# Optimization experiments

Measured on AMD Instinct MI355X. Metric: run time of the kernel, lower is better.

Reference implementation:

```python
import jax, jax.numpy as jnp
import numpy as np
from jax import lax


def setup_inputs() -> dict:
    key = jax.random.key(0)
    k1, k2 = jax.random.split(key)
    B, C = 128, 256
    z_f = jax.random.normal(k1, (B, C, 7, 7), dtype=jnp.float32)
    x_f = jax.random.normal(k2, (B, C, 31, 31), dtype=jnp.float32)
    return {"z_f": z_f, "x_f": x_f}


def xcorr_depthwise(search, kernel):
    # search: [B, C, Hx, Wx], kernel: [B, C, Hz, Wz]
    B, C, Hx, Wx = search.shape
    _, _, Hz, Wz = kernel.shape
    s = search.reshape(1, B * C, Hx, Wx)          # [1, B*C, Hx, Wx]
    k = kernel.reshape(B * C, 1, Hz, Wz)          # [B*C, 1, Hz, Wz]
    out = lax.conv_general_dilated(
        s, k,
        window_strides=(1, 1),
        padding='VALID',
        dimension_numbers=('NCHW', 'OIHW', 'NCHW'),
        feature_group_count=B * C,
    )                                             # [1, B*C, Ho, Wo]
    Ho, Wo = Hx - Hz + 1, Wx - Wz + 1
    return out.reshape(B, C, Ho, Wo)


def reference(z_f, x_f):
    # DepthwiseRPN.forward: xcorr_depthwise(search=x_f, kernel=z_f)
    return xcorr_depthwise(x_f, z_f)
```

## Files before the change

kernel.cpp:

```cpp
#include <hip/hip_runtime.h>


#define PPB 5
#define WX 31
#define XPLANE 961
#define TDW (PPB * XPLANE)
#define LPLANE 1024
#define XREG (PPB * LPLANE)
#define ZPLANE 49
#define ZDW (PPB * ZPLANE)
#define ZREG 256
#define OPLANE 625
#define WO 25

typedef __attribute__((address_space(1))) const void gaddr_t;
typedef __attribute__((address_space(3))) void laddr_t;

__global__ __launch_bounds__(128, 2) void dwxcorr_kernel(
    const float* __restrict__ z, const float* __restrict__ x,
    float* __restrict__ out, int nplanes) {
  __shared__ float lds[XREG + ZREG];

  const int tid = threadIdx.x;
  const int t = blockIdx.x;
  const int wb4 = (tid & ~63) * 4;
  const int wb1 = tid & ~63;
  const long XTOT = (long)nplanes * XPLANE;
  const long ZTOT = (long)nplanes * ZPLANE;
  const long xoff = (long)t * TDW;
  const long zoff = (long)t * ZDW;
  const long gz0 = zoff & ~3L;
  const int offz = (int)(zoff & 3);

  if (xoff + TDW + 31 <= XTOT && gz0 + ZREG <= ZTOT) {
#pragma unroll
    for (int c = 0; c < 10; ++c) {
      int s = c * 512 + tid * 4;
      int p = s >> 10;
      int row = (s >> 5) & 31;
      int q = s & 31;
      int qq = q ^ ((row & 7) << 2);
      long g = xoff + p * XPLANE + row * WX + qq;
      __builtin_amdgcn_global_load_lds((gaddr_t*)(x + g),
                                       (laddr_t*)&lds[c * 512 + wb4], 16, 0, 0);
    }
    if (tid < 63)
      __builtin_amdgcn_global_load_lds((gaddr_t*)(z + gz0 + tid * 4),
                                       (laddr_t*)&lds[XREG + wb4], 16, 0, 0);
  } else {
#pragma unroll
    for (int c = 0; c < 40; ++c) {
      int s = c * 128 + tid;
      int p = s >> 10;
      int row = (s >> 5) & 31;
      int q = s & 31;
      int qq = q ^ ((row & 7) << 2);
      long g = xoff + p * XPLANE + row * WX + qq;
      if (g > XTOT - 1) g = XTOT - 1;
      __builtin_amdgcn_global_load_lds((gaddr_t*)(x + g),
                                       (laddr_t*)&lds[c * 128 + wb1], 4, 0, 0);
    }
    if (tid < 63) {
      long gz = gz0 + tid * 4;
      if (gz > ZTOT - 4) gz = ZTOT - 4;
      __builtin_amdgcn_global_load_lds((gaddr_t*)(z + gz),
                                       (laddr_t*)&lds[XREG + wb4], 16, 0, 0);
    }
  }
  __syncthreads();

  const int p0 = t * PPB;
  const int pmax = min(PPB, nplanes - p0);
  const int cpp = tid / 25;
  if (tid >= PPB * 25 || cpp >= pmax) return;
  const int t25 = tid - cpp * 25;
  const int ty = t25 / 5;
  const int tx = t25 - ty * 5;
  const int tx5 = tx * 5;

  const float* zb = &lds[XREG + offz + cpp * ZPLANE];
  float zr[ZPLANE];
#pragma unroll
  for (int j = 0; j < ZPLANE; ++j) zr[j] = zb[j];

  float acc[5][5];
#pragma unroll
  for (int r = 0; r < 5; ++r)
#pragma unroll
    for (int j = 0; j < 5; ++j) acc[r][j] = 0.0f;

  const float* pb = &lds[cpp * LPLANE];

#pragma unroll
  for (int iy = 0; iy < 11; ++iy) {
    const int row = ty * 5 + iy;
    const int rb = row << 5;
    const int f = (row & 7) << 2;
    float xr[11];
#pragma unroll
    for (int k = 0; k < 11; ++k) xr[k] = pb[rb + ((tx5 + k) ^ f)];
    const int ky_lo = (iy - 4 < 0) ? 0 : iy - 4;
    const int ky_hi = (iy < 6) ? iy : 6;
#pragma unroll
    for (int ky = 0; ky < 7; ++ky) {
      if (ky < ky_lo || ky > ky_hi) continue;
      const int orow = iy - ky;
#pragma unroll
      for (int kx = 0; kx < 7; ++kx) {
        const float zv = zr[ky * 7 + kx];
#pragma unroll
        for (int j = 0; j < 5; ++j)
          acc[orow][j] = fmaf(xr[kx + j], zv, acc[orow][j]);
      }
    }
  }

  float* ob = out + (long)(p0 + cpp) * OPLANE + (ty * 5) * WO + tx5;
#pragma unroll
  for (int r = 0; r < 5; ++r)
#pragma unroll
    for (int j = 0; j < 5; ++j) ob[r * WO + j] = acc[r][j];
}

extern "C" void kernel_launch(void* const* d_in, const int* in_sizes, int n_in,
                              void* d_out, int out_size, void* d_ws, size_t ws_size,
                              hipStream_t stream) {
  const float* z = (const float*)d_in[0];
  const float* x = (const float*)d_in[1];
  float* out = (float*)d_out;

  const int nplanes = in_sizes[0] / ZPLANE;
  const int blocks = (nplanes + PPB - 1) / PPB;

  hipLaunchKernelGGL(dwxcorr_kernel, dim3(blocks), dim3(128), 0, stream,
                     z, x, out, nplanes);
}
```

Baseline: 45.47 us.

## Assign one full output row per thread with vectorized row loads

Each thread now computes a whole 25-wide output row instead of a 5x5 tile. It loads each of the 7 needed input rows as eight float4 LDS reads, undoing the XOR swizzle at chunk granularity. Filter weights are read from LDS per tap rather than held in 49 registers. This cuts total LDS read instructions, but threads now read full rows with more redundancy across output rows, and stores become 25 contiguous floats per thread, which may coalesce worse.

```diff
diff --git a/kernel.cpp b/kernel.cpp
--- a/kernel.cpp
+++ b/kernel.cpp
@@ -73,53 +73,40 @@
   const int pmax = min(PPB, nplanes - p0);
   const int cpp = tid / 25;
   if (tid >= PPB * 25 || cpp >= pmax) return;
-  const int t25 = tid - cpp * 25;
-  const int ty = t25 / 5;
-  const int tx = t25 - ty * 5;
-  const int tx5 = tx * 5;
+  const int oy = tid - cpp * 25;
 
   const float* zb = &lds[XREG + offz + cpp * ZPLANE];
-  float zr[ZPLANE];
+
+  float acc[25];
 #pragma unroll
-  for (int j = 0; j < ZPLANE; ++j) zr[j] = zb[j];
-
-  float acc[5][5];
-#pragma unroll
-  for (int r = 0; r < 5; ++r)
-#pragma unroll
-    for (int j = 0; j < 5; ++j) acc[r][j] = 0.0f;
-
-  const float* pb = &lds[cpp * LPLANE];
+  for (int j = 0; j < 25; ++j) acc[j] = 0.0f;
 
 #pragma unroll
-  for (int iy = 0; iy < 11; ++iy) {
-    const int row = ty * 5 + iy;
-    const int rb = row << 5;
-    const int f = (row & 7) << 2;
-    float xr[11];
+  for (int ky = 0; ky < 7; ++ky) {
+    const int row = oy + ky;
+    const int rf = row & 7;
+    const float4* rp = (const float4*)&lds[(cpp << 10) | (row << 5)];
+    float rowbuf[32];
 #pragma unroll
-    for (int k = 0; k < 11; ++k) xr[k] = pb[rb + ((tx5 + k) ^ f)];
-    const int ky_lo = (iy - 4 < 0) ? 0 : iy - 4;
-    const int ky_hi = (iy < 6) ? iy : 6;
+    for (int c = 0; c < 8; ++c) {
+      float4 v = rp[c ^ rf];
+      rowbuf[c * 4 + 0] = v.x;
+      rowbuf[c * 4 + 1] = v.y;
+      rowbuf[c * 4 + 2] = v.z;
+      rowbuf[c * 4 + 3] = v.w;
+    }
 #pragma unroll
-    for (int ky = 0; ky < 7; ++ky) {
-      if (ky < ky_lo || ky > ky_hi) continue;
-      const int orow = iy - ky;
+    for (int kx = 0; kx < 7; ++kx) {
+      const float zv = zb[ky * 7 + kx];
 #pragma unroll
-      for (int kx = 0; kx < 7; ++kx) {
-        const float zv = zr[ky * 7 + kx];
-#pragma unroll
-        for (int j = 0; j < 5; ++j)
-          acc[orow][j] = fmaf(xr[kx + j], zv, acc[orow][j]);
-      }
+      for (int ox = 0; ox < 25; ++ox)
+        acc[ox] = fmaf(rowbuf[ox + kx], zv, acc[ox]);
     }
   }
 
-  float* ob = out + (long)(p0 + cpp) * OPLANE + (ty * 5) * WO + tx5;
+  float* ob = out + (long)(p0 + cpp) * OPLANE + oy * WO;
 #pragma unroll
-  for (int r = 0; r < 5; ++r)
-#pragma unroll
-    for (int j = 0; j < 5; ++j) ob[r * WO + j] = acc[r][j];
+  for (int j = 0; j < 25; ++j) ob[j] = acc[j];
 }
 
 extern "C" void kernel_launch(void* const* d_in, const int* in_sizes, int n_in,
```

After: 56.04 us. 23.2% more time.

## Convert to persistent grid with register-staged prefetch of next tile

Applied to the files above, without the earlier changes.

Launches a fixed grid of 1792 blocks that loop over plane tiles instead of one block per tile. The next tile's x and z data are loaded from global memory into registers while the current tile is computed from LDS, then written to LDS after a barrier. The goal is to hide global load latency behind compute. The cost is 40 extra registers per thread for staging, which may hurt occupancy under launch_bounds(128,2), and it replaces the direct global-to-LDS loads with plain global loads followed by LDS stores.

```diff
diff --git a/kernel.cpp b/kernel.cpp
--- a/kernel.cpp
+++ b/kernel.cpp
@@ -12,114 +12,130 @@
 #define ZREG 256
 #define OPLANE 625
 #define WO 25
-
-typedef __attribute__((address_space(1))) const void gaddr_t;
-typedef __attribute__((address_space(3))) void laddr_t;
+#define GRID 1792
 
 __global__ __launch_bounds__(128, 2) void dwxcorr_kernel(
     const float* __restrict__ z, const float* __restrict__ x,
-    float* __restrict__ out, int nplanes) {
+    float* __restrict__ out, int nplanes, int ntiles) {
   __shared__ float lds[XREG + ZREG];
 
   const int tid = threadIdx.x;
-  const int t = blockIdx.x;
-  const int wb4 = (tid & ~63) * 4;
-  const int wb1 = tid & ~63;
   const long XTOT = (long)nplanes * XPLANE;
   const long ZTOT = (long)nplanes * ZPLANE;
-  const long xoff = (long)t * TDW;
-  const long zoff = (long)t * ZDW;
-  const long gz0 = zoff & ~3L;
-  const int offz = (int)(zoff & 3);
 
-  if (xoff + TDW + 31 <= XTOT && gz0 + ZREG <= ZTOT) {
+  int soff[10];
+#pragma unroll
+  for (int c = 0; c < 10; ++c) {
+    int s = c * 512 + tid * 4;
+    int p = s >> 10;
+    int row = (s >> 5) & 31;
+    int q = s & 31;
+    int qq = q ^ ((row & 7) << 2);
+    soff[c] = p * XPLANE + row * WX + qq;
+  }
+
+  float xrs[40];
+  float4 zr4 = make_float4(0.f, 0.f, 0.f, 0.f);
+
+  auto LOADT = [&](int t) {
+    const long xoff = (long)t * TDW;
+    const long gz0 = ((long)t * ZDW) & ~3L;
+    if (xoff + TDW + 31 <= XTOT && gz0 + ZREG <= ZTOT) {
+#pragma unroll
+      for (int c = 0; c < 10; ++c) {
+        const float* gp = x + xoff + soff[c];
+#pragma unroll
+        for (int j = 0; j < 4; ++j) xrs[c * 4 + j] = gp[j];
+      }
+      if (tid < 63) zr4 = *(const float4*)(z + gz0 + tid * 4);
+    } else {
+#pragma unroll
+      for (int c = 0; c < 10; ++c) {
+#pragma unroll
+        for (int j = 0; j < 4; ++j) {
+          long gj = xoff + soff[c] + j;
+          if (gj > XTOT - 1) gj = XTOT - 1;
+          xrs[c * 4 + j] = x[gj];
+        }
+      }
+      if (tid < 63) {
+        long gz = gz0 + tid * 4;
+        if (gz > ZTOT - 4) gz = ZTOT - 4;
+        zr4 = *(const float4*)(z + gz);
+      }
+    }
+  };
+
+  const int bstart = blockIdx.x;
+  LOADT(bstart);
+
+  for (int t = bstart; t < ntiles; t += GRID) {
+    __syncthreads();
 #pragma unroll
     for (int c = 0; c < 10; ++c) {
-      int s = c * 512 + tid * 4;
-      int p = s >> 10;
-      int row = (s >> 5) & 31;
-      int q = s & 31;
-      int qq = q ^ ((row & 7) << 2);
-      long g = xoff + p * XPLANE + row * WX + qq;
-      __builtin_amdgcn_global_load_lds((gaddr_t*)(x + g),
-                                       (laddr_t*)&lds[c * 512 + wb4], 16, 0, 0);
+      float4 v = make_float4(xrs[c * 4 + 0], xrs[c * 4 + 1],
+                             xrs[c * 4 + 2], xrs[c * 4 + 3]);
+      *(float4*)&lds[c * 512 + tid * 4] = v;
     }
-    if (tid < 63)
-      __builtin_amdgcn_global_load_lds((gaddr_t*)(z + gz0 + tid * 4),
-                                       (laddr_t*)&lds[XREG + wb4], 16, 0, 0);
-  } else {
+    if (tid < 63) *(float4*)&lds[XREG + tid * 4] = zr4;
+    __syncthreads();
+
+    const int tn = t + GRID;
+    if (tn < ntiles) LOADT(tn);
+
+    const int p0 = t * PPB;
+    const int pmax = min(PPB, nplanes - p0);
+    const int cpp = tid / 25;
+    if (tid < PPB * 25 && cpp < pmax) {
+      const int t25 = tid - cpp * 25;
+      const int ty = t25 / 5;
+      const int tx = t25 - ty * 5;
+      const int tx5 = tx * 5;
+      const int offz = (int)(((long)t * ZDW) & 3);
+
+      const float* zb = &lds[XREG + offz + cpp * ZPLANE];
+      float zr[ZPLANE];
 #pragma unroll
-    for (int c = 0; c < 40; ++c) {
-      int s = c * 128 + tid;
-      int p = s >> 10;
-      int row = (s >> 5) & 31;
-      int q = s & 31;
-      int qq = q ^ ((row & 7) << 2);
-      long g = xoff + p * XPLANE + row * WX + qq;
-      if (g > XTOT - 1) g = XTOT - 1;
-      __builtin_amdgcn_global_load_lds((gaddr_t*)(x + g),
-                                       (laddr_t*)&lds[c * 128 + wb1], 4, 0, 0);
-    }
-    if (tid < 63) {
-      long gz = gz0 + tid * 4;
-      if (gz > ZTOT - 4) gz = ZTOT - 4;
-      __builtin_amdgcn_global_load_lds((gaddr_t*)(z + gz),
-                                       (laddr_t*)&lds[XREG + wb4], 16, 0, 0);
+      for (int j = 0; j < ZPLANE; ++j) zr[j] = zb[j];
+
+      float acc[5][5];
+#pragma unroll
+      for (int r = 0; r < 5; ++r)
+#pragma unroll
+        for (int j2 = 0; j2 < 5; ++j2) acc[r][j2] = 0.0f;
+
+      const float* pb = &lds[cpp * LPLANE];
+#pragma unroll
+      for (int iy = 0; iy < 11; ++iy) {
+        const int row = ty * 5 + iy;
+        const int rb = row << 5;
+        const int f = (row & 7) << 2;
+        float xr[11];
+#pragma unroll
+        for (int k = 0; k < 11; ++k) xr[k] = pb[rb + ((tx5 + k) ^ f)];
+        const int ky_lo = (iy - 4 < 0) ? 0 : iy - 4;
+        const int ky_hi = (iy < 6) ? iy : 6;
+#pragma unroll
+        for (int ky = 0; ky < 7; ++ky) {
+          if (ky < ky_lo || ky > ky_hi) continue;
+          const int orow = iy - ky;
+#pragma unroll
+          for (int kx = 0; kx < 7; ++kx) {
+            const float zv = zr[ky * 7 + kx];
+#pragma unroll
+            for (int j2 = 0; j2 < 5; ++j2)
+              acc[orow][j2] = fmaf(xr[kx + j2], zv, acc[orow][j2]);
+          }
+        }
+      }
+
+      float* ob = out + (long)(p0 + cpp) * OPLANE + (ty * 5) * WO + tx5;
+#pragma unroll
+      for (int r = 0; r < 5; ++r)
+#pragma unroll
+        for (int j2 = 0; j2 < 5; ++j2) ob[r * WO + j2] = acc[r][j2];
     }
   }
-  __syncthreads();
-
-  const int p0 = t * PPB;
-  const int pmax = min(PPB, nplanes - p0);
-  const int cpp = tid / 25;
-  if (tid >= PPB * 25 || cpp >= pmax) return;
-  const int t25 = tid - cpp * 25;
-  const int ty = t25 / 5;
-  const int tx = t25 - ty * 5;
-  const int tx5 = tx * 5;
-
-  const float* zb = &lds[XREG + offz + cpp * ZPLANE];
-  float zr[ZPLANE];
-#pragma unroll
-  for (int j = 0; j < ZPLANE; ++j) zr[j] = zb[j];
-
-  float acc[5][5];
-#pragma unroll
-  for (int r = 0; r < 5; ++r)
-#pragma unroll
-    for (int j = 0; j < 5; ++j) acc[r][j] = 0.0f;
-
-  const float* pb = &lds[cpp * LPLANE];
-
-#pragma unroll
-  for (int iy = 0; iy < 11; ++iy) {
-    const int row = ty * 5 + iy;
-    const int rb = row << 5;
-    const int f = (row & 7) << 2;
-    float xr[11];
-#pragma unroll
-    for (int k = 0; k < 11; ++k) xr[k] = pb[rb + ((tx5 + k) ^ f)];
-    const int ky_lo = (iy - 4 < 0) ? 0 : iy - 4;
-    const int ky_hi = (iy < 6) ? iy : 6;
-#pragma unroll
-    for (int ky = 0; ky < 7; ++ky) {
-      if (ky < ky_lo || ky > ky_hi) continue;
-      const int orow = iy - ky;
-#pragma unroll
-      for (int kx = 0; kx < 7; ++kx) {
-        const float zv = zr[ky * 7 + kx];
-#pragma unroll
-        for (int j = 0; j < 5; ++j)
-          acc[orow][j] = fmaf(xr[kx + j], zv, acc[orow][j]);
-      }
-    }
-  }
-
-  float* ob = out + (long)(p0 + cpp) * OPLANE + (ty * 5) * WO + tx5;
-#pragma unroll
-  for (int r = 0; r < 5; ++r)
-#pragma unroll
-    for (int j = 0; j < 5; ++j) ob[r * WO + j] = acc[r][j];
 }
 
 extern "C" void kernel_launch(void* const* d_in, const int* in_sizes, int n_in,
@@ -130,8 +146,8 @@
   float* out = (float*)d_out;
 
   const int nplanes = in_sizes[0] / ZPLANE;
-  const int blocks = (nplanes + PPB - 1) / PPB;
+  const int ntiles = (nplanes + PPB - 1) / PPB;
 
-  hipLaunchKernelGGL(dwxcorr_kernel, dim3(blocks), dim3(128), 0, stream,
-                     z, x, out, nplanes);
+  hipLaunchKernelGGL(dwxcorr_kernel, dim3(GRID), dim3(128), 0, stream,
+                     z, x, out, nplanes, ntiles);
 }
```

Measured after the change: 127.9 us. 181% more time.
